# Kernel optimization log

Measured on AMD Instinct MI355X. Metric: run time of the kernel, lower is better.

## Reference

```python
import jax, jax.numpy as jnp
import numpy as np

P_DROP = 0.31881923790897965  # torch.dropout p from the original module


def setup_inputs() -> dict:
    key = jax.random.key(0)
    k1, k2, k3, k4 = jax.random.split(key, 4)
    B, H, S, KV, D = 1, 16, 2048, 4096, 64  # KV = 2*S so the [S,2S] triu|tril mask lines up
    query = jax.random.normal(k1, (B, H, S, D), dtype=jnp.float32)
    key_t = jax.random.normal(k2, (B, H, KV, D), dtype=jnp.float32)
    value = jax.random.normal(k3, (B, H, KV, D), dtype=jnp.float32)
    # deterministic dropout keep-mask, keep prob = 1 - p
    drop_mask = jax.random.bernoulli(k4, 1.0 - P_DROP, (B, H, S, KV))
    return {"query": query, "key": key_t, "value": value, "drop_mask": drop_mask}


def _structured_mask(S, dtype):
    # torch.cat([triu(ones(S,S,bool),1), tril(ones(S,S,bool))], dim=-1) -> [S, 2S]
    # bool mask is ADDED to scores (promotes to 0/1 floats), exactly as in the original.
    triu = jnp.triu(jnp.ones((S, S), dtype=bool), 1)
    tril = jnp.tril(jnp.ones((S, S), dtype=bool))
    return jnp.concatenate([triu, tril], axis=-1).astype(dtype)  # [S, 2S]


def reference(query, key, value, drop_mask):
    B, H, S, D = query.shape
    scale = jnp.asarray(1.0 / np.sqrt(D), query.dtype)
    mask = _structured_mask(S, query.dtype)  # [S, 2S] of 0/1
    # qk: [B,H,S,KV]
    qk = jnp.einsum('bhsd,bhkd->bhsk', query, key) * scale + mask
    attn = jax.nn.softmax(qk, axis=-1)
    keep_scale = jnp.asarray(1.0 / (1.0 - P_DROP), attn.dtype)
    attn = jnp.where(drop_mask, attn * keep_scale, jnp.zeros((), attn.dtype))
    return jnp.einsum('bhsk,bhkd->bhsd', attn, value)
```

## Files before the change

### kernel.cpp

```cpp
#include <hip/hip_runtime.h>
#include <hip/hip_bf16.h>


#define H_   16
#define S_   2048
#define KV_  4096
#define D_   64
#define NSPLIT 2
#define CPB  32

using bf16x8 = __attribute__((ext_vector_type(8))) __bf16;
using f32x4  = __attribute__((ext_vector_type(4))) float;
using f32x16 = __attribute__((ext_vector_type(16))) float;
using uintx4 = __attribute__((ext_vector_type(4))) unsigned;

constexpr float KEEP_SCALE = (float)(1.0 / (1.0 - 0.31881923790897965));
#define C_SC  0.18033688011112043f
#define C_ONE -10.098865286222744f
#define C_ZRO -11.541560327111707f

#define WS_FLAG 0
#define WS_K    256
#define WS_V    (WS_K + 8388608)
#define WS_PART (WS_V + 8388608)
#define WS_LS   (WS_PART + 16777216)

__device__ __forceinline__ bf16x8 as_bf16x8(uintx4 v) {
    bf16x8 r; __builtin_memcpy(&r, &v, 16); return r;
}
__device__ __forceinline__ void gld16(const void* g, void* l) {
    __builtin_amdgcn_global_load_lds(
        (const __attribute__((address_space(1))) unsigned*)g,
        (__attribute__((address_space(3))) unsigned*)l, 16, 0, 0);
}

__global__ void detect_mask(const unsigned* __restrict__ m, int* __restrict__ flag) {
    __shared__ int bad;
    if (threadIdx.x == 0) bad = 0;
    __syncthreads();
    int ok = 1;
    for (int i = threadIdx.x; i < 4096; i += blockDim.x) {
        unsigned w = m[i];
        if (w > 1u && w != 0x3F800000u) ok = 0;
    }
    if (!ok) atomicOr(&bad, 1);
    __syncthreads();
    if (threadIdx.x == 0) *flag = bad;
}

__global__ __launch_bounds__(256)
void conv_kv(const float* __restrict__ K, const float* __restrict__ V,
             char* __restrict__ kt, char* __restrict__ vt) {
    __shared__ __bf16 Ks[64][72];
    __shared__ __bf16 Vs[64][72];
    const int hc = blockIdx.x;
    const int h = hc >> 6, c = hc & 63;
    const int tid = threadIdx.x;
    const float* ksrc = K + ((size_t)h * KV_ + c * 64) * D_;
    const float* vsrc = V + ((size_t)h * KV_ + c * 64) * D_;
    #pragma unroll
    for (int it = 0; it < 4; ++it) {
        const int f = it * 1024 + tid * 4;
        const int row = f >> 6, col = f & 63;
        f32x4 a = *(const f32x4*)(ksrc + f);
        f32x4 v = *(const f32x4*)(vsrc + f);
        #pragma unroll
        for (int e = 0; e < 4; ++e) {
            Ks[row][col + e] = (__bf16)a[e];
            Vs[col + e][row] = (__bf16)v[e];
        }
    }
    __syncthreads();
    char* kdst = kt + (size_t)hc * 8192;
    char* vdst = vt + (size_t)hc * 8192;
    #pragma unroll
    for (int r = 0; r < 2; ++r) {
        const int u = r * 256 + tid;
        const int g8 = u >> 6, l = u & 63;
        const int lo = l & 31, hi = l >> 5;
        const int aa = g8 >> 2, bb = g8 & 3;
        *(bf16x8*)(kdst + u * 16) = *(const bf16x8*)&Ks[aa * 32 + lo][bb * 16 + hi * 8];
        *(bf16x8*)(vdst + u * 16) = *(const bf16x8*)&Vs[aa * 32 + lo][bb * 16 + hi * 8];
    }
}

__global__ __launch_bounds__(256, 2)
void attn_fwd(const float* __restrict__ Q,
              const unsigned char* __restrict__ Mb,
              const int* __restrict__ flagp,
              const char* __restrict__ Ktiles,
              const char* __restrict__ Vtiles,
              float* __restrict__ Part,
              float* __restrict__ Ls)
{
    __shared__ char smem[32768];

    const int tid  = threadIdx.x;
    const int wave = tid >> 6, lane = tid & 63;
    const int lo   = lane & 31, hi = lane >> 5;

    const int b  = blockIdx.x;
    const int wg = (b & 7) * 64 + (b >> 3);
    const int h  = wg >> 5;
    const int rr = wg & 31, split = rr >> 4, qt = rr & 15;
    const int q0w = qt * 128 + wave * 32;
    const int q_g = q0w + lo;

    const bool byteMode = (*flagp != 0);
    const unsigned* Mw = (const unsigned*)Mb;

    bf16x8 bq[4];
    {
        const float* qrow = Q + ((size_t)h * S_ + q_g) * D_;
        #pragma unroll
        for (int dt = 0; dt < 4; ++dt) {
            f32x4 f0 = *(const f32x4*)(qrow + dt * 16 + hi * 8);
            f32x4 f1 = *(const f32x4*)(qrow + dt * 16 + hi * 8 + 4);
            bf16x8 bb;
            #pragma unroll
            for (int e = 0; e < 4; ++e) { bb[e] = (__bf16)f0[e]; bb[4 + e] = (__bf16)f1[e]; }
            bq[dt] = bb;
        }
    }

    const char* gK = Ktiles + (size_t)h * 64 * 8192;
    const char* gV = Vtiles + (size_t)h * 64 * 8192;
    float lsum = 0.f;
    f32x16 acc0 = {}, acc1 = {};

    auto stage = [&](int buf, int c) {
        const char* sk = gK + (size_t)c * 8192 + tid * 16;
        const char* sv = gV + (size_t)c * 8192 + tid * 16;
        char* dk = smem + buf * 16384 + tid * 16;
        gld16(sk,        dk);
        gld16(sk + 4096, dk + 4096);
        gld16(sv,        dk + 8192);
        gld16(sv + 4096, dk + 12288);
    };

    unsigned mreg[32];
    auto load_bits = [&](int cc) {
        if (byteMode) {
            const unsigned char* base = Mb + ((size_t)h * S_ + q0w) * KV_ + (size_t)cc * 64 + lane;
            #pragma unroll
            for (int i = 0; i < 32; ++i) mreg[i] = base[(size_t)i * KV_];
        } else {
            const unsigned* base = Mw + ((size_t)h * S_ + q0w) * KV_ + (size_t)cc * 64 + lane;
            #pragma unroll
            for (int i = 0; i < 32; ++i) mreg[i] = base[(size_t)i * KV_];
        }
    };
    auto ballot_bits = [&]() -> unsigned long long {
        unsigned long long sav = 0;
        #pragma unroll
        for (int i = 0; i < 32; ++i) {
            unsigned long long bal = __ballot(mreg[i] != 0u);
            if ((lane & 31) == i) sav = bal;
        }
        return sav;
    };

    const int cs = split * CPB, ce = cs + CPB;
    load_bits(cs);
    stage(0, cs);
    unsigned long long mb_cur = ballot_bits();
    __syncthreads();
    int cur = 0;

    for (int c = cs; c < ce; ++c) {
        const bool more = (c + 1 < ce);
        if (more) load_bits(c + 1);
        if (more) stage(cur ^ 1, c + 1);
        const unsigned long long mb = mb_cur;
        const char* Kb = smem + cur * 16384;
        const char* Vb = Kb + 8192;

        f32x16 st0 = {}, st1 = {};
        __builtin_amdgcn_s_setprio(1);
        #pragma unroll
        for (int dt = 0; dt < 4; ++dt) {
            bf16x8 k0 = *(const bf16x8*)(Kb + ((dt)     * 64 + lane) * 16);
            bf16x8 k1 = *(const bf16x8*)(Kb + ((4 + dt) * 64 + lane) * 16);
            st0 = __builtin_amdgcn_mfma_f32_32x32x16_bf16(k0, bq[dt], st0, 0, 0, 0);
            st1 = __builtin_amdgcn_mfma_f32_32x32x16_bf16(k1, bq[dt], st1, 0, 0, 0);
        }
        __builtin_amdgcn_s_setprio(0);

        bf16x8 pf[4];
        #pragma unroll
        for (int kvt = 0; kvt < 2; ++kvt) {
            float pd[16];
            #pragma unroll
            for (int r = 0; r < 16; ++r) {
                const float sv = kvt ? st1[r] : st0[r];
                const int kvl = kvt * 32 + (r & 3) + 8 * (r >> 2) + 4 * hi;
                const int kvg = c * 64 + kvl;
                const bool one = (kvg < S_) ? (kvg > q_g) : (kvg - S_ <= q_g);
                float v = fmaf(sv, C_SC, one ? C_ONE : C_ZRO);
                float pp = exp2f(v);
                lsum += pp;
                pd[r] = ((mb >> kvl) & 1) ? pp : 0.f;
            }
            unsigned pk[8], X[8];
            #pragma unroll
            for (int j = 0; j < 8; ++j) {
                unsigned t;
                asm("v_cvt_pk_bf16_f32 %0, %1, %2" : "=v"(t) : "v"(pd[2 * j]), "v"(pd[2 * j + 1]));
                pk[j] = t;
            }
            #pragma unroll
            for (int j = 0; j < 8; ++j) X[j] = (unsigned)__shfl_xor((int)pk[j], 32);
            uintx4 f0, f1;
            if (hi) {
                f0 = (uintx4){X[2], X[3], pk[2], pk[3]};
                f1 = (uintx4){X[6], X[7], pk[6], pk[7]};
            } else {
                f0 = (uintx4){pk[0], pk[1], X[0], X[1]};
                f1 = (uintx4){pk[4], pk[5], X[4], X[5]};
            }
            pf[kvt * 2]     = as_bf16x8(f0);
            pf[kvt * 2 + 1] = as_bf16x8(f1);
        }

        __builtin_amdgcn_s_setprio(1);
        #pragma unroll
        for (int kvk = 0; kvk < 4; ++kvk) {
            bf16x8 v0 = *(const bf16x8*)(Vb + ((kvk)     * 64 + lane) * 16);
            bf16x8 v1 = *(const bf16x8*)(Vb + ((4 + kvk) * 64 + lane) * 16);
            acc0 = __builtin_amdgcn_mfma_f32_32x32x16_bf16(pf[kvk], v0, acc0, 0, 0, 0);
            acc1 = __builtin_amdgcn_mfma_f32_32x32x16_bf16(pf[kvk], v1, acc1, 0, 0, 0);
        }
        __builtin_amdgcn_s_setprio(0);

        if (more) mb_cur = ballot_bits();

        __syncthreads();
        cur ^= 1;
    }

    lsum += __shfl_xor(lsum, 32);
    if (hi == 0) Ls[((size_t)split * H_ + h) * S_ + q_g] = lsum;
    float* pa = Part + ((size_t)split * H_ + h) * S_ * 64;
    #pragma unroll
    for (int r = 0; r < 16; ++r) {
        const int q = q0w + (r & 3) + 8 * (r >> 2) + 4 * hi;
        __builtin_nontemporal_store(acc0[r], pa + (size_t)q * 64 + lo);
        __builtin_nontemporal_store(acc1[r], pa + (size_t)q * 64 + 32 + lo);
    }
}

__global__ __launch_bounds__(256)
void combine(const float* __restrict__ Part, const float* __restrict__ Ls,
             float* __restrict__ Out) {
    const int idx = blockIdx.x * 256 + threadIdx.x;
    const int r  = idx >> 4;
    const int dg = (idx & 15) * 4;
    const f32x4 a = *(const f32x4*)(Part + (size_t)r * D_ + dg);
    const f32x4 b = *(const f32x4*)(Part + (size_t)(H_ * S_ + r) * D_ + dg);
    const float l = Ls[r] + Ls[H_ * S_ + r];
    const float s = KEEP_SCALE / l;
    f32x4 o;
    #pragma unroll
    for (int e = 0; e < 4; ++e) o[e] = (a[e] + b[e]) * s;
    *(f32x4*)(Out + (size_t)r * D_ + dg) = o;
}

extern "C" void kernel_launch(void* const* d_in, const int* in_sizes, int n_in,
                              void* d_out, int out_size, void* d_ws, size_t ws_size,
                              hipStream_t stream) {
    const float* Q = (const float*)d_in[0];
    const float* K = (const float*)d_in[1];
    const float* V = (const float*)d_in[2];
    const unsigned char* M = (const unsigned char*)d_in[3];
    char* ws = (char*)d_ws;
    int* flag = (int*)(ws + WS_FLAG);
    char* kt = ws + WS_K;
    char* vt = ws + WS_V;
    float* part = (float*)(ws + WS_PART);
    float* ls = (float*)(ws + WS_LS);

    detect_mask<<<1, 256, 0, stream>>>((const unsigned*)M, flag);
    conv_kv<<<1024, 256, 0, stream>>>(K, V, kt, vt);
    attn_fwd<<<512, 256, 0, stream>>>(Q, M, flag, kt, vt, part, ls);
    combine<<<2048, 256, 0, stream>>>(part, ls, (float*)d_out);
}
```

Measured before the change: 182.6 us.

## Split KV four ways, interleave QK and PV per subtile, raise occupancy

```diff
diff --git a/kernel.cpp b/kernel.cpp
--- a/kernel.cpp
+++ b/kernel.cpp
@@ -6,8 +6,8 @@
 #define S_   2048
 #define KV_  4096
 #define D_   64
-#define NSPLIT 2
-#define CPB  32
+#define NSPLIT 4
+#define CPB  16
 
 using bf16x8 = __attribute__((ext_vector_type(8))) __bf16;
 using f32x4  = __attribute__((ext_vector_type(4))) float;
@@ -23,7 +23,7 @@
 #define WS_K    256
 #define WS_V    (WS_K + 8388608)
 #define WS_PART (WS_V + 8388608)
-#define WS_LS   (WS_PART + 16777216)
+#define WS_LS   (WS_PART + 33554432)
 
 __device__ __forceinline__ bf16x8 as_bf16x8(uintx4 v) {
     bf16x8 r; __builtin_memcpy(&r, &v, 16); return r;
@@ -84,7 +84,7 @@
     }
 }
 
-__global__ __launch_bounds__(256, 2)
+__global__ __launch_bounds__(256, 4)
 void attn_fwd(const float* __restrict__ Q,
               const unsigned char* __restrict__ Mb,
               const int* __restrict__ flagp,
@@ -100,9 +100,9 @@
     const int lo   = lane & 31, hi = lane >> 5;
 
     const int b  = blockIdx.x;
-    const int wg = (b & 7) * 64 + (b >> 3);
-    const int h  = wg >> 5;
-    const int rr = wg & 31, split = rr >> 4, qt = rr & 15;
+    const int wg = (b & 7) * 128 + (b >> 3);
+    const int h  = wg >> 6;
+    const int rr = wg & 63, split = rr >> 4, qt = rr & 15;
     const int q0w = qt * 128 + wave * 32;
     const int q_g = q0w + lo;
 
@@ -175,28 +175,24 @@
         const char* Kb = smem + cur * 16384;
         const char* Vb = Kb + 8192;
 
-        f32x16 st0 = {}, st1 = {};
-        __builtin_amdgcn_s_setprio(1);
-        #pragma unroll
-        for (int dt = 0; dt < 4; ++dt) {
-            bf16x8 k0 = *(const bf16x8*)(Kb + ((dt)     * 64 + lane) * 16);
-            bf16x8 k1 = *(const bf16x8*)(Kb + ((4 + dt) * 64 + lane) * 16);
-            st0 = __builtin_amdgcn_mfma_f32_32x32x16_bf16(k0, bq[dt], st0, 0, 0, 0);
-            st1 = __builtin_amdgcn_mfma_f32_32x32x16_bf16(k1, bq[dt], st1, 0, 0, 0);
-        }
-        __builtin_amdgcn_s_setprio(0);
-
-        bf16x8 pf[4];
         #pragma unroll
         for (int kvt = 0; kvt < 2; ++kvt) {
+            f32x16 st = {};
+            __builtin_amdgcn_s_setprio(1);
+            #pragma unroll
+            for (int dt = 0; dt < 4; ++dt) {
+                bf16x8 kfr = *(const bf16x8*)(Kb + ((kvt * 4 + dt) * 64 + lane) * 16);
+                st = __builtin_amdgcn_mfma_f32_32x32x16_bf16(kfr, bq[dt], st, 0, 0, 0);
+            }
+            __builtin_amdgcn_s_setprio(0);
+
             float pd[16];
             #pragma unroll
             for (int r = 0; r < 16; ++r) {
-                const float sv = kvt ? st1[r] : st0[r];
                 const int kvl = kvt * 32 + (r & 3) + 8 * (r >> 2) + 4 * hi;
                 const int kvg = c * 64 + kvl;
                 const bool one = (kvg < S_) ? (kvg > q_g) : (kvg - S_ <= q_g);
-                float v = fmaf(sv, C_SC, one ? C_ONE : C_ZRO);
+                float v = fmaf(st[r], C_SC, one ? C_ONE : C_ZRO);
                 float pp = exp2f(v);
                 lsum += pp;
                 pd[r] = ((mb >> kvl) & 1) ? pp : 0.f;
@@ -218,19 +214,21 @@
                 f0 = (uintx4){pk[0], pk[1], X[0], X[1]};
                 f1 = (uintx4){pk[4], pk[5], X[4], X[5]};
             }
-            pf[kvt * 2]     = as_bf16x8(f0);
-            pf[kvt * 2 + 1] = as_bf16x8(f1);
-        }
-
-        __builtin_amdgcn_s_setprio(1);
-        #pragma unroll
-        for (int kvk = 0; kvk < 4; ++kvk) {
-            bf16x8 v0 = *(const bf16x8*)(Vb + ((kvk)     * 64 + lane) * 16);
-            bf16x8 v1 = *(const bf16x8*)(Vb + ((4 + kvk) * 64 + lane) * 16);
-            acc0 = __builtin_amdgcn_mfma_f32_32x32x16_bf16(pf[kvk], v0, acc0, 0, 0, 0);
-            acc1 = __builtin_amdgcn_mfma_f32_32x32x16_bf16(pf[kvk], v1, acc1, 0, 0, 0);
-        }
-        __builtin_amdgcn_s_setprio(0);
+            bf16x8 pf0 = as_bf16x8(f0);
+            bf16x8 pf1 = as_bf16x8(f1);
+
+            __builtin_amdgcn_s_setprio(1);
+            #pragma unroll
+            for (int j = 0; j < 2; ++j) {
+                const int kvk = kvt * 2 + j;
+                bf16x8 pfj = j ? pf1 : pf0;
+                bf16x8 v0 = *(const bf16x8*)(Vb + ((kvk)     * 64 + lane) * 16);
+                bf16x8 v1 = *(const bf16x8*)(Vb + ((4 + kvk) * 64 + lane) * 16);
+                acc0 = __builtin_amdgcn_mfma_f32_32x32x16_bf16(pfj, v0, acc0, 0, 0, 0);
+                acc1 = __builtin_amdgcn_mfma_f32_32x32x16_bf16(pfj, v1, acc1, 0, 0, 0);
+            }
+            __builtin_amdgcn_s_setprio(0);
+        }
 
         if (more) mb_cur = ballot_bits();
 
@@ -255,13 +253,19 @@
     const int idx = blockIdx.x * 256 + threadIdx.x;
     const int r  = idx >> 4;
     const int dg = (idx & 15) * 4;
-    const f32x4 a = *(const f32x4*)(Part + (size_t)r * D_ + dg);
-    const f32x4 b = *(const f32x4*)(Part + (size_t)(H_ * S_ + r) * D_ + dg);
-    const float l = Ls[r] + Ls[H_ * S_ + r];
-    const float s = KEEP_SCALE / l;
+    f32x4 s = {0.f, 0.f, 0.f, 0.f};
+    float l = 0.f;
+    #pragma unroll
+    for (int sp = 0; sp < NSPLIT; ++sp) {
+        const f32x4 a = *(const f32x4*)(Part + ((size_t)sp * H_ * S_ + r) * D_ + dg);
+        #pragma unroll
+        for (int e = 0; e < 4; ++e) s[e] += a[e];
+        l += Ls[(size_t)sp * H_ * S_ + r];
+    }
+    const float k = KEEP_SCALE / l;
     f32x4 o;
     #pragma unroll
-    for (int e = 0; e < 4; ++e) o[e] = (a[e] + b[e]) * s;
+    for (int e = 0; e < 4; ++e) o[e] = s[e] * k;
     *(f32x4*)(Out + (size_t)r * D_ + dg) = o;
 }
 
@@ -281,6 +285,6 @@
 
     detect_mask<<<1, 256, 0, stream>>>((const unsigned*)M, flag);
     conv_kv<<<1024, 256, 0, stream>>>(K, V, kt, vt);
-    attn_fwd<<<512, 256, 0, stream>>>(Q, M, flag, kt, vt, part, ls);
+    attn_fwd<<<1024, 256, 0, stream>>>(Q, M, flag, kt, vt, part, ls);
     combine<<<2048, 256, 0, stream>>>(part, ls, (float*)d_out);
 }
```

New measurement: 728.2 us. +298.7%, slower.
